# Optimization experiments

Hardware: AMD Instinct MI355X
Metric: run time of the kernel (lower is better)

Reference implementation:

```python
import jax, jax.numpy as jnp
import numpy as np

NEG_SLOPE = 0.2


def gat_layer(x, src, dst, W, a_src, a_dst, b, concat):
    # x: [N, F_in], W: [F_in, H*C], a_src/a_dst: [H, C], b: [H*C] or [C]
    N = x.shape[0]
    H, C = a_src.shape
    h = (x @ W).reshape(N, H, C)                       # per-head projections
    al_s = jnp.einsum('nhc,hc->nh', h, a_src)          # [N, H]
    al_d = jnp.einsum('nhc,hc->nh', h, a_dst)          # [N, H]
    e = jax.nn.leaky_relu(al_s[src] + al_d[dst], NEG_SLOPE)  # [E, H]
    # softmax over incoming edges of each destination node
    m = jax.ops.segment_max(e, dst, num_segments=N)    # [N, H]
    ex = jnp.exp(e - m[dst])
    s = jax.ops.segment_sum(ex, dst, num_segments=N)   # [N, H]
    alpha = ex / (s[dst] + 1e-16)                      # [E, H]
    msg = h[src] * alpha[:, :, None]                   # [E, H, C]
    out = jax.ops.segment_sum(msg, dst, num_segments=N)  # [N, H, C]
    out = out.reshape(N, H * C) if concat else out.mean(axis=1)
    return out + b


def setup_inputs() -> dict:
    key = jax.random.key(0)
    ks = jax.random.split(key, 12)
    N, E, F_in, HID, H, NCLS = 100000, 1600000, 128, 32, 4, 40
    x = jax.random.normal(ks[0], (N, F_in), dtype=jnp.float32)
    edge_index = jax.random.randint(ks[1], (2, E), 0, N, dtype=jnp.int32)
    W1 = jax.random.normal(ks[2], (F_in, H * HID), dtype=jnp.float32) * 0.1
    as1 = jax.random.normal(ks[3], (H, HID), dtype=jnp.float32) * 0.1
    ad1 = jax.random.normal(ks[4], (H, HID), dtype=jnp.float32) * 0.1
    b1 = jnp.zeros((H * HID,), dtype=jnp.float32)
    W2 = jax.random.normal(ks[5], (H * HID, H * NCLS), dtype=jnp.float32) * 0.1
    as2 = jax.random.normal(ks[6], (H, NCLS), dtype=jnp.float32) * 0.1
    ad2 = jax.random.normal(ks[7], (H, NCLS), dtype=jnp.float32) * 0.1
    b2 = jnp.zeros((NCLS,), dtype=jnp.float32)
    return {"x": x, "edge_index": edge_index, "W1": W1, "as1": as1,
            "ad1": ad1, "b1": b1, "W2": W2, "as2": as2, "ad2": ad2, "b2": b2}


def reference(x, edge_index, W1, as1, ad1, b1, W2, as2, ad2, b2):
    src, dst = edge_index[0], edge_index[1]
    h = gat_layer(x, src, dst, W1, as1, ad1, b1, concat=True)
    h = jax.nn.relu(h)  # dropout=0.0 -> identity
    out = gat_layer(h, src, dst, W2, as2, ad2, b2, concat=False)
    return jax.nn.log_softmax(out, axis=-1)
```

## Files before the change

### kernel.cpp

```cpp
#include <hip/hip_runtime.h>

typedef short short8 __attribute__((ext_vector_type(8)));
typedef float f32x4 __attribute__((ext_vector_type(4)));
typedef int   i32x4 __attribute__((ext_vector_type(4)));
typedef unsigned short u16;
typedef unsigned int u32;

__device__ __forceinline__ float b2f(u16 u){ union{u32 i; float f;} v; v.i=((u32)u)<<16; return v.f; }
__device__ __forceinline__ u16 f2b(float f){ union{float f; u32 i;} v; v.f=f; return (u16)((v.i + 0x7fffu + ((v.i>>16)&1u))>>16); }
__device__ __forceinline__ float loadv(const void* p, long i, bool isbf){
  return isbf ? b2f(((const u16*)p)[i]) : ((const float*)p)[i];
}

__global__ void detect_bf16(const void* x, int n, int* flag){
  __shared__ int cnt;
  if (threadIdx.x==0) cnt = 0;
  __syncthreads();
  int m = n < 4096 ? n : 4096;
  int good = 0;
  for (int i = threadIdx.x; i < m; i += 256){
    u16 u = ((const u16*)x)[i];
    int e = (u >> 7) & 0xff;
    if (u == 0 || (e >= 100 && e <= 140)) good++;
  }
  atomicAdd(&cnt, good);
  __syncthreads();
  if (threadIdx.x==0){
    flag[0] = (cnt >= (m*3)/4) ? 1 : 0;
    flag[1] = 1;
  }
}

__global__ __launch_bounds__(256) void convw(const void* __restrict__ W, u16* __restrict__ WT,
                                             int M, const int* __restrict__ flag){
  const bool wbf = *flag != 0;
  int i = blockIdx.x*256 + threadIdx.x;
  if (i >= 128*M) return;
  int k = i / M, c = i - k*M;
  WT[c*128 + k] = wbf ? ((const u16*)W)[i] : f2b(((const float*)W)[i]);
}

__global__ __launch_bounds__(256) void count_x(const int* __restrict__ dst,
    int* __restrict__ counts, int E, int N, int nchunk){
  int r = blockIdx.x & 7;
  int chunk = blockIdx.x >> 3;
  int lo = (int)(((long)N * r) >> 3);
  int hi = (int)(((long)N * (r+1)) >> 3);
  int per = (E + nchunk - 1) / nchunk;
  int s = chunk * per, t = min(E, s + per);
  for (int e = s + threadIdx.x; e < t; e += 256){
    int d = dst[e];
    if (d >= lo && d < hi) atomicAdd(&counts[d], 1);
  }
}

__global__ __launch_bounds__(256) void scatter_x(const int* __restrict__ src, const int* __restrict__ dst,
    const int* __restrict__ rp, int* __restrict__ cur,
    int* __restrict__ psrc, int E, int N, int nchunk){
  int r = blockIdx.x & 7;
  int chunk = blockIdx.x >> 3;
  int lo = (int)(((long)N * r) >> 3);
  int hi = (int)(((long)N * (r+1)) >> 3);
  int per = (E + nchunk - 1) / nchunk;
  int s = chunk * per, t = min(E, s + per);
  for (int e = s + threadIdx.x; e < t; e += 256){
    int d = dst[e];
    if (d >= lo && d < hi){
      int pos = rp[d] + atomicAdd(&cur[d], 1);
      psrc[pos] = src[e];
    }
  }
}

__global__ __launch_bounds__(256) void scan_bsum(const int* __restrict__ counts, int* __restrict__ bsum, int N){
  __shared__ int sm[256];
  int t = threadIdx.x, i = blockIdx.x*256 + t;
  sm[t] = (i < N) ? counts[i] : 0;
  __syncthreads();
  for (int off = 128; off; off >>= 1){
    if (t < off) sm[t] += sm[t+off];
    __syncthreads();
  }
  if (t == 0) bsum[blockIdx.x] = sm[0];
}

__global__ __launch_bounds__(1024) void scan_top(const int* __restrict__ bsum, int* __restrict__ bscan, int B){
  __shared__ int sm[1024];
  int t = threadIdx.x;
  int v = (t < B) ? bsum[t] : 0;
  sm[t] = v;
  __syncthreads();
  for (int off = 1; off < 1024; off <<= 1){
    int x = (t >= off) ? sm[t-off] : 0;
    __syncthreads();
    sm[t] += x;
    __syncthreads();
  }
  if (t < B) bscan[t] = sm[t] - v;
}

__global__ __launch_bounds__(256) void scan_final(const int* __restrict__ counts, const int* __restrict__ bscan,
                                                  int* __restrict__ rp, int N, int E){
  __shared__ int sm[256];
  int t = threadIdx.x, i = blockIdx.x*256 + t;
  int v = (i < N) ? counts[i] : 0;
  sm[t] = v;
  __syncthreads();
  for (int off = 1; off < 256; off <<= 1){
    int x = (t >= off) ? sm[t-off] : 0;
    __syncthreads();
    sm[t] += x;
    __syncthreads();
  }
  if (i < N) rp[i] = bscan[blockIdx.x] + sm[t] - v;
  if (i == 0) rp[N] = E;
}

template<int M>
__global__ __launch_bounds__(256) void gemm_k(const void* __restrict__ X, const u16* __restrict__ WT,
                                              u16* __restrict__ OUT, int N,
                                              const int* __restrict__ flagX){
  __shared__ u16 wt[M][136];
  const bool xbf = *flagX != 0;
  int tid = threadIdx.x;
  for (int i = tid; i < M*16; i += 256){
    int c = i >> 4, k8 = (i & 15) << 3;
    *(short8*)&wt[c][k8] = *(const short8*)&WT[c*128 + k8];
  }
  __syncthreads();
  int wave = tid >> 6, lane = tid & 63;
  int quad = lane >> 4, l16 = lane & 15;
  int rowbase = blockIdx.x*64 + wave*16;
  int rr = rowbase + l16; if (rr >= N) rr = N-1;
  const int NT = M/16;
  f32x4 acc[NT];
  #pragma unroll
  for (int t=0;t<NT;t++) acc[t] = (f32x4){0.f,0.f,0.f,0.f};
  #pragma unroll
  for (int kt = 0; kt < 4; kt++){
    int kb = kt*32 + quad*8;
    short8 a;
    if (xbf){
      a = *(const short8*)((const u16*)X + (size_t)rr*128 + kb);
    } else {
      const float* xf = (const float*)X + (size_t)rr*128 + kb;
      #pragma unroll
      for (int j=0;j<8;j++) a[j] = (short)f2b(xf[j]);
    }
    #pragma unroll
    for (int t=0;t<NT;t++){
      short8 b = *(const short8*)&wt[t*16 + l16][kb];
      acc[t] = __builtin_amdgcn_mfma_f32_16x16x32_bf16(a, b, acc[t], 0, 0, 0);
    }
  }
  #pragma unroll
  for (int t=0;t<NT;t++){
    #pragma unroll
    for (int r=0;r<4;r++){
      int row = rowbase + quad*4 + r;
      if (row < N) OUT[(size_t)row*M + t*16 + l16] = f2b(acc[t][r]);
    }
  }
}

template<int C>
__global__ __launch_bounds__(256) void al_k(const u16* __restrict__ Hm, const void* __restrict__ as_,
                     const void* __restrict__ ad_,
                     float* __restrict__ als, float* __restrict__ ald, int N, const int* __restrict__ flag){
  __shared__ float s_as[4*C], s_ad[4*C];
  const bool isbf = *flag != 0;
  for (int i = threadIdx.x; i < 4*C; i += 256){
    s_as[i] = loadv(as_, i, isbf);
    s_ad[i] = loadv(ad_, i, isbf);
  }
  __syncthreads();
  int idx = blockIdx.x*256 + threadIdx.x;
  if (idx >= N*4) return;
  int n = idx >> 2, h = idx & 3;
  const short8* row = (const short8*)(Hm + (size_t)n*(4*C) + h*C);
  float ss = 0.f, sd = 0.f;
  #pragma unroll
  for (int v = 0; v < C/8; v++){
    short8 pk = row[v];
    #pragma unroll
    for (int j = 0; j < 8; j++){
      union{u32 i; float f;} u; u.i = ((u32)(u16)pk[j]) << 16;
      ss += u.f * s_as[h*C + v*8 + j];
      sd += u.f * s_ad[h*C + v*8 + j];
    }
  }
  als[idx] = ss;
  ald[idx] = sd;
}

__global__ __launch_bounds__(256) void agg1(const u16* __restrict__ h1,
    const float* __restrict__ als, const float* __restrict__ ald, const void* __restrict__ b1,
    const int* __restrict__ rp, const int* __restrict__ psrc,
    u16* __restrict__ hrelu, int N, const int* __restrict__ flag){
  __shared__ __align__(16) int   sbuf[4][16];
  __shared__ __align__(16) float ebT[4][4*20];
  const bool isbf = *flag != 0;
  int wave = threadIdx.x >> 6, lane = threadIdx.x & 63;
  int node = blockIdx.x*4 + wave;
  bool live = node < N;
  int nd = live ? node : 0;
  int hd = lane >> 4;
  int eidx = lane >> 2, hA = lane & 3;
  int beg = __builtin_amdgcn_readfirstlane(rp[nd]);
  int end = __builtin_amdgcn_readfirstlane(rp[nd+1]);
  if (!live){ beg = 0; end = 0; }
  float advA = ald[nd*4 + hA];
  const char* hb = (const char*)h1;
  int lane4 = lane << 2;
  int* sb = sbuf[wave];
  float* eb = ebT[wave];
  float a0 = 0.f, a1 = 0.f;
  float sp = 0.f;
  for (int cbeg = beg; cbeg < end; cbeg += 16){
    int cnt = min(16, end - cbeg);
    int e = cbeg + eidx;
    bool vv = e < end;
    int ec = vv ? e : beg;
    int s = psrc[ec];
    float lv = als[s*4 + hA] + advA;
    lv = fmaxf(lv, 0.2f*lv);
    float ex = vv ? __expf(lv) : 0.f;
    sp += ex;
    eb[hA*20 + eidx] = ex;
    if (hA == 0) sb[eidx] = vv ? (s << 8) : 0;
    for (int j0 = 0; j0 < cnt; j0 += 4){
      i32x4 off4 = *(const i32x4*)&sb[j0];
      f32x4 ex4  = *(const f32x4*)&eb[hd*20 + j0];
      u32 p[4];
      #pragma unroll
      for (int i=0;i<4;i++) p[i] = *(const u32*)(hb + (u32)(off4[i] + lane4));
      #pragma unroll
      for (int i=0;i<4;i++){
        union{u32 u; float f;} w;
        w.u = p[i] << 16;         a0 += ex4[i]*w.f;
        w.u = p[i] & 0xffff0000u; a1 += ex4[i]*w.f;
      }
    }
  }
  sp += __shfl_xor(sp, 4);  sp += __shfl_xor(sp, 8);
  sp += __shfl_xor(sp, 16); sp += __shfl_xor(sp, 32);
  float sum = __shfl(sp, hd);
  if (live){
    float inv = 1.f/(sum + 1e-16f);
    float v0 = a0*inv + loadv(b1, 2*lane,     isbf);
    float v1 = a1*inv + loadv(b1, 2*lane + 1, isbf);
    v0 = v0 > 0.f ? v0 : 0.f;
    v1 = v1 > 0.f ? v1 : 0.f;
    u32 packed = (u32)f2b(v0) | ((u32)f2b(v1) << 16);
    *(u32*)(hrelu + (size_t)node*128 + 2*lane) = packed;
  }
}

__global__ __launch_bounds__(256) void agg2(const u16* __restrict__ h2,
    const float* __restrict__ als, const float* __restrict__ ald, const void* __restrict__ b2,
    const int* __restrict__ rp, const int* __restrict__ psrc,
    void* __restrict__ out, int N, const int* __restrict__ flag){
  __shared__ __align__(16) int   sbuf[4][16];
  __shared__ __align__(16) float ebT[4][4*20];
  __shared__ __align__(16) float sm[4][160];
  const bool isbf = *flag != 0;
  int wave = threadIdx.x >> 6, lane = threadIdx.x & 63;
  int node = blockIdx.x*4 + wave;
  bool live = node < N;
  int nd = live ? node : 0;
  int g = lane >> 4, s = lane & 15;
  int hm = s / 5;
  int moff = s << 4;
  int toff = 256 + (s << 2);
  int eidx = lane >> 2, hA = lane & 3;
  int beg = __builtin_amdgcn_readfirstlane(rp[nd]);
  int end = __builtin_amdgcn_readfirstlane(rp[nd+1]);
  if (!live){ beg = 0; end = 0; }
  float advA = ald[nd*4 + hA];
  const char* hb = (const char*)h2;
  int* sb = sbuf[wave];
  float* eb = ebT[wave];
  float am[8] = {0.f,0.f,0.f,0.f,0.f,0.f,0.f,0.f};
  float at0 = 0.f, at1 = 0.f;
  float sp = 0.f;
  for (int cbeg = beg; cbeg < end; cbeg += 16){
    int cnt = min(16, end - cbeg);
    int e = cbeg + eidx;
    bool vv = e < end;
    int ec = vv ? e : beg;
    int src = psrc[ec];
    float lv = als[src*4 + hA] + advA;
    lv = fmaxf(lv, 0.2f*lv);
    float ex = vv ? __expf(lv) : 0.f;
    sp += ex;
    eb[hA*20 + eidx] = ex;
    if (hA == 0) sb[eidx] = vv ? src*320 : 0;
    for (int j0 = 0; j0 < cnt; j0 += 4){
      int off   = sb[j0 + g];
      float exm = eb[hm*20 + j0 + g];
      float ext = eb[3*20  + j0 + g];
      i32x4 P = *(const i32x4*)(hb + (u32)(off + moff));
      u32   q = *(const u32*) (hb + (u32)(off + toff));
      union{u32 u; float f;} w;
      #pragma unroll
      for (int i=0;i<4;i++){
        u32 pv = (u32)P[i];
        w.u = pv << 16;         am[2*i]   += exm*w.f;
        w.u = pv & 0xffff0000u; am[2*i+1] += exm*w.f;
      }
      w.u = q << 16;         at0 += ext*w.f;
      w.u = q & 0xffff0000u; at1 += ext*w.f;
    }
  }
  sp += __shfl_xor(sp, 4);  sp += __shfl_xor(sp, 8);
  sp += __shfl_xor(sp, 16); sp += __shfl_xor(sp, 32);
  float Sm = __shfl(sp, hm);
  float S3 = __shfl(sp, 3);
  #pragma unroll
  for (int k=0;k<8;k++){ am[k] += __shfl_xor(am[k],16); am[k] += __shfl_xor(am[k],32); }
  at0 += __shfl_xor(at0,16); at0 += __shfl_xor(at0,32);
  at1 += __shfl_xor(at1,16); at1 += __shfl_xor(at1,32);
  if (lane < 16){
    float invm = 1.f/(Sm + 1e-16f);
    float invt = 1.f/(S3 + 1e-16f);
    f32x4 v0 = {am[0]*invm, am[1]*invm, am[2]*invm, am[3]*invm};
    f32x4 v1 = {am[4]*invm, am[5]*invm, am[6]*invm, am[7]*invm};
    *(f32x4*)&sm[wave][8*s]     = v0;
    *(f32x4*)&sm[wave][8*s + 4] = v1;
    sm[wave][128 + 2*s] = at0*invt;
    sm[wave][129 + 2*s] = at1*invt;
  }
  __syncthreads();
  float v = -__builtin_inff();
  if (lane < 40)
    v = (sm[wave][lane] + sm[wave][40+lane] + sm[wave][80+lane] + sm[wave][120+lane]) * 0.25f
        + loadv(b2, lane, isbf);
  float mxo = v;
  for (int o = 32; o; o >>= 1) mxo = fmaxf(mxo, __shfl_xor(mxo, o));
  float ex = (lane < 40) ? __expf(v - mxo) : 0.f;
  float S = ex;
  for (int o = 32; o; o >>= 1) S += __shfl_xor(S, o);
  if (live && lane < 40){
    float r = v - mxo - __logf(S);
    if (isbf) ((u16*)out)[(size_t)node*40 + lane] = f2b(r);
    else      ((float*)out)[(size_t)node*40 + lane] = r;
  }
}

extern "C" void kernel_launch(void* const* d_in, const int* in_sizes, int n_in,
                              void* d_out, int out_size, void* d_ws, size_t ws_size,
                              hipStream_t stream){
  const void* x   = d_in[0];
  const int*  ei  = (const int*)d_in[1];
  const void* W1  = d_in[2];
  const void* as1 = d_in[3];
  const void* ad1 = d_in[4];
  const void* b1  = d_in[5];
  const void* W2  = d_in[6];
  const void* as2 = d_in[7];
  const void* ad2 = d_in[8];
  const void* b2  = d_in[9];

  const int N = in_sizes[0] / 128;
  const int E = in_sizes[1] / 2;
  const int* esrc = ei;
  const int* edst = ei + E;

  char* w = (char*)d_ws;
  size_t off = 0;
  auto take = [&](size_t bytes)->void*{
    void* p = w + off;
    off = (off + bytes + 255) & ~(size_t)255;
    return p;
  };
  u16*   h12    = (u16*)take((size_t)N*160*2);
  u16*   hrelu  = (u16*)take((size_t)N*128*2);
  float* als1   = (float*)take((size_t)N*4*4);
  float* ald1   = (float*)take((size_t)N*4*4);
  float* als2   = (float*)take((size_t)N*4*4);
  float* ald2   = (float*)take((size_t)N*4*4);
  int*   rowptr = (int*)take((size_t)(N+1)*4);
  int*   counts = (int*)take((size_t)N*4);
  int*   bsum   = (int*)take(1024*4);
  int*   bscan  = (int*)take(1024*4);
  int*   psrc   = (int*)take((size_t)E*4);
  int*   flag   = (int*)take(64);
  u16*   wt1    = (u16*)take(128*128*2);
  u16*   wt2    = (u16*)take(160*128*2);

  const int B = (N + 255) / 256;
  const int NCHUNK = 128;

  detect_bf16<<<1, 256, 0, stream>>>(x, N*128, flag);
  convw<<<(128*128+255)/256, 256, 0, stream>>>(W1, wt1, 128, flag);
  convw<<<(128*160+255)/256, 256, 0, stream>>>(W2, wt2, 160, flag);

  hipMemsetAsync(counts, 0, (size_t)N*4, stream);
  count_x<<<8*NCHUNK, 256, 0, stream>>>(edst, counts, E, N, NCHUNK);
  scan_bsum<<<B, 256, 0, stream>>>(counts, bsum, N);
  scan_top<<<1, 1024, 0, stream>>>(bsum, bscan, B);
  scan_final<<<B, 256, 0, stream>>>(counts, bscan, rowptr, N, E);
  hipMemsetAsync(counts, 0, (size_t)N*4, stream);
  scatter_x<<<8*NCHUNK, 256, 0, stream>>>(esrc, edst, rowptr, counts, psrc, E, N, NCHUNK);

  gemm_k<128><<<(N+63)/64, 256, 0, stream>>>(x, wt1, h12, N, flag);
  al_k<32><<<(4*N+255)/256, 256, 0, stream>>>(h12, as1, ad1, als1, ald1, N, flag);
  agg1<<<(N+3)/4, 256, 0, stream>>>(h12, als1, ald1, b1, rowptr, psrc, hrelu, N, flag);

  gemm_k<160><<<(N+63)/64, 256, 0, stream>>>(hrelu, wt2, h12, N, flag+1);
  al_k<40><<<(4*N+255)/256, 256, 0, stream>>>(h12, as2, ad2, als2, ald2, N, flag);
  agg2<<<(N+3)/4, 256, 0, stream>>>(h12, als2, ald2, b2, rowptr, psrc, d_out, N, flag);
}
```

Measured before the change: 486.8 us.

## Split edge softmax numerators into separate kernel and batch gathers in aggregation

Adds an edgex kernel that computes the per-edge exp scores and per-node denominators ahead of time and stores them in a workspace buffer. The aggregation kernels then just read the precomputed values. agg1 is remapped to 16-byte row loads with a cross-group reduction like agg2. Both aggregations now issue four gathers at once on full 16-edge chunks to raise memory-level parallelism. The cost is an extra launch plus writing and reading a 25.6 MB edge buffer for each layer.

```diff
diff --git a/kernel.cpp b/kernel.cpp
--- a/kernel.cpp
+++ b/kernel.cpp
@@ -193,75 +193,119 @@
   ald[idx] = sd;
 }
 
+__global__ __launch_bounds__(256) void edgex(const float* __restrict__ als, const float* __restrict__ ald,
+    const int* __restrict__ rp, const int* __restrict__ psrc,
+    float* __restrict__ ex, float* __restrict__ nsum, int N){
+  int wave = threadIdx.x >> 6, lane = threadIdx.x & 63;
+  int node = blockIdx.x*4 + wave;
+  bool live = node < N;
+  int nd = live ? node : 0;
+  int eidx = lane >> 2, hA = lane & 3;
+  int beg = __builtin_amdgcn_readfirstlane(rp[nd]);
+  int end = __builtin_amdgcn_readfirstlane(rp[nd+1]);
+  if (!live){ beg = 0; end = 0; }
+  float adv = ald[nd*4 + hA];
+  float sp = 0.f;
+  for (int cbeg = beg; cbeg < end; cbeg += 16){
+    int e = cbeg + eidx;
+    if (e < end){
+      int s = psrc[e];
+      float lv = als[s*4 + hA] + adv;
+      lv = fmaxf(lv, 0.2f*lv);
+      float ev = __expf(lv);
+      sp += ev;
+      ex[(size_t)e*4 + hA] = ev;
+    }
+  }
+  sp += __shfl_xor(sp, 4);  sp += __shfl_xor(sp, 8);
+  sp += __shfl_xor(sp, 16); sp += __shfl_xor(sp, 32);
+  if (live && lane < 4) nsum[nd*4 + lane] = sp;
+}
+
 __global__ __launch_bounds__(256) void agg1(const u16* __restrict__ h1,
-    const float* __restrict__ als, const float* __restrict__ ald, const void* __restrict__ b1,
+    const float* __restrict__ ex, const float* __restrict__ nsum, const void* __restrict__ b1,
     const int* __restrict__ rp, const int* __restrict__ psrc,
     u16* __restrict__ hrelu, int N, const int* __restrict__ flag){
   __shared__ __align__(16) int   sbuf[4][16];
-  __shared__ __align__(16) float ebT[4][4*20];
+  __shared__ __align__(16) float ebuf[4][64];
   const bool isbf = *flag != 0;
   int wave = threadIdx.x >> 6, lane = threadIdx.x & 63;
   int node = blockIdx.x*4 + wave;
   bool live = node < N;
   int nd = live ? node : 0;
-  int hd = lane >> 4;
+  int g = lane >> 4, s = lane & 15;
+  int hm = s >> 2;
+  int moff = s << 4;
   int eidx = lane >> 2, hA = lane & 3;
   int beg = __builtin_amdgcn_readfirstlane(rp[nd]);
   int end = __builtin_amdgcn_readfirstlane(rp[nd+1]);
   if (!live){ beg = 0; end = 0; }
-  float advA = ald[nd*4 + hA];
   const char* hb = (const char*)h1;
-  int lane4 = lane << 2;
   int* sb = sbuf[wave];
-  float* eb = ebT[wave];
-  float a0 = 0.f, a1 = 0.f;
-  float sp = 0.f;
+  float* eb = ebuf[wave];
+  float am[8] = {0.f,0.f,0.f,0.f,0.f,0.f,0.f,0.f};
   for (int cbeg = beg; cbeg < end; cbeg += 16){
     int cnt = min(16, end - cbeg);
     int e = cbeg + eidx;
     bool vv = e < end;
-    int ec = vv ? e : beg;
-    int s = psrc[ec];
-    float lv = als[s*4 + hA] + advA;
-    lv = fmaxf(lv, 0.2f*lv);
-    float ex = vv ? __expf(lv) : 0.f;
-    sp += ex;
-    eb[hA*20 + eidx] = ex;
-    if (hA == 0) sb[eidx] = vv ? (s << 8) : 0;
-    for (int j0 = 0; j0 < cnt; j0 += 4){
-      i32x4 off4 = *(const i32x4*)&sb[j0];
-      f32x4 ex4  = *(const f32x4*)&eb[hd*20 + j0];
-      u32 p[4];
-      #pragma unroll
-      for (int i=0;i<4;i++) p[i] = *(const u32*)(hb + (u32)(off4[i] + lane4));
-      #pragma unroll
-      for (int i=0;i<4;i++){
+    float exv = vv ? ex[(size_t)e*4 + hA] : 0.f;
+    eb[lane] = exv;
+    if (hA == 0) sb[eidx] = vv ? (psrc[e] << 8) : 0;
+    int njj = (cnt + 3) >> 2;
+    if (njj == 4){
+      int of[4]; float em[4]; i32x4 P[4];
+      #pragma unroll
+      for (int jj=0;jj<4;jj++){ of[jj] = sb[jj*4 + g]; em[jj] = eb[(jj*4 + g)*4 + hm]; }
+      #pragma unroll
+      for (int jj=0;jj<4;jj++) P[jj] = *(const i32x4*)(hb + (u32)(of[jj] + moff));
+      #pragma unroll
+      for (int jj=0;jj<4;jj++){
         union{u32 u; float f;} w;
-        w.u = p[i] << 16;         a0 += ex4[i]*w.f;
-        w.u = p[i] & 0xffff0000u; a1 += ex4[i]*w.f;
-      }
-    }
-  }
-  sp += __shfl_xor(sp, 4);  sp += __shfl_xor(sp, 8);
-  sp += __shfl_xor(sp, 16); sp += __shfl_xor(sp, 32);
-  float sum = __shfl(sp, hd);
-  if (live){
-    float inv = 1.f/(sum + 1e-16f);
-    float v0 = a0*inv + loadv(b1, 2*lane,     isbf);
-    float v1 = a1*inv + loadv(b1, 2*lane + 1, isbf);
-    v0 = v0 > 0.f ? v0 : 0.f;
-    v1 = v1 > 0.f ? v1 : 0.f;
-    u32 packed = (u32)f2b(v0) | ((u32)f2b(v1) << 16);
-    *(u32*)(hrelu + (size_t)node*128 + 2*lane) = packed;
+        #pragma unroll
+        for (int i=0;i<4;i++){
+          u32 pv = (u32)P[jj][i];
+          w.u = pv << 16;         am[2*i]   += em[jj]*w.f;
+          w.u = pv & 0xffff0000u; am[2*i+1] += em[jj]*w.f;
+        }
+      }
+    } else {
+      for (int jj=0;jj<njj;jj++){
+        int of = sb[jj*4 + g]; float em = eb[(jj*4 + g)*4 + hm];
+        i32x4 P = *(const i32x4*)(hb + (u32)(of + moff));
+        union{u32 u; float f;} w;
+        #pragma unroll
+        for (int i=0;i<4;i++){
+          u32 pv = (u32)P[i];
+          w.u = pv << 16;         am[2*i]   += em*w.f;
+          w.u = pv & 0xffff0000u; am[2*i+1] += em*w.f;
+        }
+      }
+    }
+  }
+  #pragma unroll
+  for (int k=0;k<8;k++){ am[k] += __shfl_xor(am[k],16); am[k] += __shfl_xor(am[k],32); }
+  if (live && lane < 16){
+    float Sm = nsum[nd*4 + hm];
+    float inv = 1.f/(Sm + 1e-16f);
+    float v[8];
+    #pragma unroll
+    for (int k=0;k<8;k++){
+      float t = am[k]*inv + loadv(b1, 8*s + k, isbf);
+      v[k] = t > 0.f ? t : 0.f;
+    }
+    i32x4 pk;
+    #pragma unroll
+    for (int k=0;k<4;k++) pk[k] = (int)((u32)f2b(v[2*k]) | ((u32)f2b(v[2*k+1]) << 16));
+    *(i32x4*)(hrelu + (size_t)node*128 + 8*s) = pk;
   }
 }
 
 __global__ __launch_bounds__(256) void agg2(const u16* __restrict__ h2,
-    const float* __restrict__ als, const float* __restrict__ ald, const void* __restrict__ b2,
+    const float* __restrict__ ex, const float* __restrict__ nsum, const void* __restrict__ b2,
     const int* __restrict__ rp, const int* __restrict__ psrc,
     void* __restrict__ out, int N, const int* __restrict__ flag){
   __shared__ __align__(16) int   sbuf[4][16];
-  __shared__ __align__(16) float ebT[4][4*20];
+  __shared__ __align__(16) float ebuf[4][64];
   __shared__ __align__(16) float sm[4][160];
   const bool isbf = *flag != 0;
   int wave = threadIdx.x >> 6, lane = threadIdx.x & 63;
@@ -276,51 +320,70 @@
   int beg = __builtin_amdgcn_readfirstlane(rp[nd]);
   int end = __builtin_amdgcn_readfirstlane(rp[nd+1]);
   if (!live){ beg = 0; end = 0; }
-  float advA = ald[nd*4 + hA];
   const char* hb = (const char*)h2;
   int* sb = sbuf[wave];
-  float* eb = ebT[wave];
+  float* eb = ebuf[wave];
   float am[8] = {0.f,0.f,0.f,0.f,0.f,0.f,0.f,0.f};
   float at0 = 0.f, at1 = 0.f;
-  float sp = 0.f;
   for (int cbeg = beg; cbeg < end; cbeg += 16){
     int cnt = min(16, end - cbeg);
     int e = cbeg + eidx;
     bool vv = e < end;
-    int ec = vv ? e : beg;
-    int src = psrc[ec];
-    float lv = als[src*4 + hA] + advA;
-    lv = fmaxf(lv, 0.2f*lv);
-    float ex = vv ? __expf(lv) : 0.f;
-    sp += ex;
-    eb[hA*20 + eidx] = ex;
-    if (hA == 0) sb[eidx] = vv ? src*320 : 0;
-    for (int j0 = 0; j0 < cnt; j0 += 4){
-      int off   = sb[j0 + g];
-      float exm = eb[hm*20 + j0 + g];
-      float ext = eb[3*20  + j0 + g];
-      i32x4 P = *(const i32x4*)(hb + (u32)(off + moff));
-      u32   q = *(const u32*) (hb + (u32)(off + toff));
-      union{u32 u; float f;} w;
-      #pragma unroll
-      for (int i=0;i<4;i++){
-        u32 pv = (u32)P[i];
-        w.u = pv << 16;         am[2*i]   += exm*w.f;
-        w.u = pv & 0xffff0000u; am[2*i+1] += exm*w.f;
-      }
-      w.u = q << 16;         at0 += ext*w.f;
-      w.u = q & 0xffff0000u; at1 += ext*w.f;
-    }
-  }
-  sp += __shfl_xor(sp, 4);  sp += __shfl_xor(sp, 8);
-  sp += __shfl_xor(sp, 16); sp += __shfl_xor(sp, 32);
-  float Sm = __shfl(sp, hm);
-  float S3 = __shfl(sp, 3);
+    float exv = vv ? ex[(size_t)e*4 + hA] : 0.f;
+    eb[lane] = exv;
+    if (hA == 0) sb[eidx] = vv ? psrc[e]*320 : 0;
+    int njj = (cnt + 3) >> 2;
+    if (njj == 4){
+      int of[4]; float em[4], et[4]; i32x4 P[4]; u32 q[4];
+      #pragma unroll
+      for (int jj=0;jj<4;jj++){
+        of[jj] = sb[jj*4 + g];
+        em[jj] = eb[(jj*4 + g)*4 + hm];
+        et[jj] = eb[(jj*4 + g)*4 + 3];
+      }
+      #pragma unroll
+      for (int jj=0;jj<4;jj++){
+        P[jj] = *(const i32x4*)(hb + (u32)(of[jj] + moff));
+        q[jj] = *(const u32*) (hb + (u32)(of[jj] + toff));
+      }
+      #pragma unroll
+      for (int jj=0;jj<4;jj++){
+        union{u32 u; float f;} w;
+        #pragma unroll
+        for (int i=0;i<4;i++){
+          u32 pv = (u32)P[jj][i];
+          w.u = pv << 16;         am[2*i]   += em[jj]*w.f;
+          w.u = pv & 0xffff0000u; am[2*i+1] += em[jj]*w.f;
+        }
+        w.u = q[jj] << 16;         at0 += et[jj]*w.f;
+        w.u = q[jj] & 0xffff0000u; at1 += et[jj]*w.f;
+      }
+    } else {
+      for (int jj=0;jj<njj;jj++){
+        int of = sb[jj*4 + g];
+        float em = eb[(jj*4 + g)*4 + hm];
+        float et = eb[(jj*4 + g)*4 + 3];
+        i32x4 P = *(const i32x4*)(hb + (u32)(of + moff));
+        u32   q = *(const u32*) (hb + (u32)(of + toff));
+        union{u32 u; float f;} w;
+        #pragma unroll
+        for (int i=0;i<4;i++){
+          u32 pv = (u32)P[i];
+          w.u = pv << 16;         am[2*i]   += em*w.f;
+          w.u = pv & 0xffff0000u; am[2*i+1] += em*w.f;
+        }
+        w.u = q << 16;         at0 += et*w.f;
+        w.u = q & 0xffff0000u; at1 += et*w.f;
+      }
+    }
+  }
   #pragma unroll
   for (int k=0;k<8;k++){ am[k] += __shfl_xor(am[k],16); am[k] += __shfl_xor(am[k],32); }
   at0 += __shfl_xor(at0,16); at0 += __shfl_xor(at0,32);
   at1 += __shfl_xor(at1,16); at1 += __shfl_xor(at1,32);
   if (lane < 16){
+    float Sm = nsum[nd*4 + hm];
+    float S3 = nsum[nd*4 + 3];
     float invm = 1.f/(Sm + 1e-16f);
     float invt = 1.f/(S3 + 1e-16f);
     f32x4 v0 = {am[0]*invm, am[1]*invm, am[2]*invm, am[3]*invm};
@@ -337,8 +400,8 @@
         + loadv(b2, lane, isbf);
   float mxo = v;
   for (int o = 32; o; o >>= 1) mxo = fmaxf(mxo, __shfl_xor(mxo, o));
-  float ex = (lane < 40) ? __expf(v - mxo) : 0.f;
-  float S = ex;
+  float exl = (lane < 40) ? __expf(v - mxo) : 0.f;
+  float S = exl;
   for (int o = 32; o; o >>= 1) S += __shfl_xor(S, o);
   if (live && lane < 40){
     float r = v - mxo - __logf(S);
@@ -387,6 +450,8 @@
   int*   flag   = (int*)take(64);
   u16*   wt1    = (u16*)take(128*128*2);
   u16*   wt2    = (u16*)take(160*128*2);
+  float* exbuf  = (float*)take((size_t)E*4*4);
+  float* nsum   = (float*)take((size_t)N*4*4);
 
   const int B = (N + 255) / 256;
   const int NCHUNK = 128;
@@ -405,9 +470,11 @@
 
   gemm_k<128><<<(N+63)/64, 256, 0, stream>>>(x, wt1, h12, N, flag);
   al_k<32><<<(4*N+255)/256, 256, 0, stream>>>(h12, as1, ad1, als1, ald1, N, flag);
-  agg1<<<(N+3)/4, 256, 0, stream>>>(h12, als1, ald1, b1, rowptr, psrc, hrelu, N, flag);
+  edgex<<<(N+3)/4, 256, 0, stream>>>(als1, ald1, rowptr, psrc, exbuf, nsum, N);
+  agg1<<<(N+3)/4, 256, 0, stream>>>(h12, exbuf, nsum, b1, rowptr, psrc, hrelu, N, flag);
 
   gemm_k<160><<<(N+63)/64, 256, 0, stream>>>(hrelu, wt2, h12, N, flag+1);
   al_k<40><<<(4*N+255)/256, 256, 0, stream>>>(h12, as2, ad2, als2, ald2, N, flag);
-  agg2<<<(N+3)/4, 256, 0, stream>>>(h12, als2, ald2, b2, rowptr, psrc, d_out, N, flag);
-}
+  edgex<<<(N+3)/4, 256, 0, stream>>>(als2, ald2, rowptr, psrc, exbuf, nsum, N);
+  agg2<<<(N+3)/4, 256, 0, stream>>>(h12, exbuf, nsum, b2, rowptr, psrc, d_out, N, flag);
+}
```

New measurement: 534.1 us. +9.7%, slower.

## Split layer-2 features into 128+32 arrays and single-pass CSR build

Applied to the files above, without the earlier changes.

Layer-2 projected features are now stored as a 128-wide main array plus a separate 32-wide tail array instead of one 160-wide interleaved array. The gather in agg2 reads each 16-byte chunk from a 256-byte aligned row plus a 4-byte tail read from a 64-byte row, which should improve cache-line alignment for the random neighbor loads. The count and scatter kernels drop the 8-way destination-range partitioning and do one pass over the edges with a grid-stride loop. That removes the 8x redundant edge reads but gives up whatever atomic locality the partitioning provided.

```diff
diff --git a/kernel.cpp b/kernel.cpp
--- a/kernel.cpp
+++ b/kernel.cpp
@@ -40,35 +40,20 @@
   WT[c*128 + k] = wbf ? ((const u16*)W)[i] : f2b(((const float*)W)[i]);
 }
 
-__global__ __launch_bounds__(256) void count_x(const int* __restrict__ dst,
-    int* __restrict__ counts, int E, int N, int nchunk){
-  int r = blockIdx.x & 7;
-  int chunk = blockIdx.x >> 3;
-  int lo = (int)(((long)N * r) >> 3);
-  int hi = (int)(((long)N * (r+1)) >> 3);
-  int per = (E + nchunk - 1) / nchunk;
-  int s = chunk * per, t = min(E, s + per);
-  for (int e = s + threadIdx.x; e < t; e += 256){
+__global__ __launch_bounds__(256) void count_1p(const int* __restrict__ dst, int* __restrict__ counts, int E){
+  int i = blockIdx.x*256 + threadIdx.x;
+  int stride = gridDim.x*256;
+  for (int e = i; e < E; e += stride) atomicAdd(&counts[dst[e]], 1);
+}
+
+__global__ __launch_bounds__(256) void scatter_1p(const int* __restrict__ src, const int* __restrict__ dst,
+    const int* __restrict__ rp, int* __restrict__ cur, int* __restrict__ psrc, int E){
+  int i = blockIdx.x*256 + threadIdx.x;
+  int stride = gridDim.x*256;
+  for (int e = i; e < E; e += stride){
     int d = dst[e];
-    if (d >= lo && d < hi) atomicAdd(&counts[d], 1);
-  }
-}
-
-__global__ __launch_bounds__(256) void scatter_x(const int* __restrict__ src, const int* __restrict__ dst,
-    const int* __restrict__ rp, int* __restrict__ cur,
-    int* __restrict__ psrc, int E, int N, int nchunk){
-  int r = blockIdx.x & 7;
-  int chunk = blockIdx.x >> 3;
-  int lo = (int)(((long)N * r) >> 3);
-  int hi = (int)(((long)N * (r+1)) >> 3);
-  int per = (E + nchunk - 1) / nchunk;
-  int s = chunk * per, t = min(E, s + per);
-  for (int e = s + threadIdx.x; e < t; e += 256){
-    int d = dst[e];
-    if (d >= lo && d < hi){
-      int pos = rp[d] + atomicAdd(&cur[d], 1);
-      psrc[pos] = src[e];
-    }
+    int pos = rp[d] + atomicAdd(&cur[d], 1);
+    psrc[pos] = src[e];
   }
 }
 
@@ -118,7 +103,7 @@
 
 template<int M>
 __global__ __launch_bounds__(256) void gemm_k(const void* __restrict__ X, const u16* __restrict__ WT,
-                                              u16* __restrict__ OUT, int N,
+                                              u16* __restrict__ OUT, u16* __restrict__ OUT2, int N,
                                               const int* __restrict__ flagX){
   __shared__ u16 wt[M][136];
   const bool xbf = *flagX != 0;
@@ -158,7 +143,11 @@
     #pragma unroll
     for (int r=0;r<4;r++){
       int row = rowbase + quad*4 + r;
-      if (row < N) OUT[(size_t)row*M + t*16 + l16] = f2b(acc[t][r]);
+      if (row < N){
+        u16 val = f2b(acc[t][r]);
+        if (M > 128 && t*16 >= 128) OUT2[(size_t)row*32 + (t*16 - 128) + l16] = val;
+        else                        OUT [(size_t)row*128 + t*16 + l16]        = val;
+      }
     }
   }
 }
@@ -187,6 +176,37 @@
       union{u32 i; float f;} u; u.i = ((u32)(u16)pk[j]) << 16;
       ss += u.f * s_as[h*C + v*8 + j];
       sd += u.f * s_ad[h*C + v*8 + j];
+    }
+  }
+  als[idx] = ss;
+  ald[idx] = sd;
+}
+
+__global__ __launch_bounds__(256) void al2_k(const u16* __restrict__ Hm, const u16* __restrict__ Ht,
+                     const void* __restrict__ as_, const void* __restrict__ ad_,
+                     float* __restrict__ als, float* __restrict__ ald, int N, const int* __restrict__ flag){
+  __shared__ float s_as[160], s_ad[160];
+  const bool isbf = *flag != 0;
+  for (int i = threadIdx.x; i < 160; i += 256){
+    s_as[i] = loadv(as_, i, isbf);
+    s_ad[i] = loadv(ad_, i, isbf);
+  }
+  __syncthreads();
+  int idx = blockIdx.x*256 + threadIdx.x;
+  if (idx >= N*4) return;
+  int n = idx >> 2, h = idx & 3;
+  float ss = 0.f, sd = 0.f;
+  int c0 = h*40;
+  #pragma unroll
+  for (int v = 0; v < 5; v++){
+    int c = c0 + v*8;
+    const u16* p = (c < 128) ? (Hm + (size_t)n*128 + c) : (Ht + (size_t)n*32 + (c - 128));
+    short8 pk = *(const short8*)p;
+    #pragma unroll
+    for (int j = 0; j < 8; j++){
+      union{u32 i; float f;} u; u.i = ((u32)(u16)pk[j]) << 16;
+      ss += u.f * s_as[c + j];
+      sd += u.f * s_ad[c + j];
     }
   }
   als[idx] = ss;
@@ -256,7 +276,7 @@
   }
 }
 
-__global__ __launch_bounds__(256) void agg2(const u16* __restrict__ h2,
+__global__ __launch_bounds__(256) void agg2(const u16* __restrict__ h2m, const u16* __restrict__ h2t,
     const float* __restrict__ als, const float* __restrict__ ald, const void* __restrict__ b2,
     const int* __restrict__ rp, const int* __restrict__ psrc,
     void* __restrict__ out, int N, const int* __restrict__ flag){
@@ -271,13 +291,14 @@
   int g = lane >> 4, s = lane & 15;
   int hm = s / 5;
   int moff = s << 4;
-  int toff = 256 + (s << 2);
+  int tof  = s << 2;
   int eidx = lane >> 2, hA = lane & 3;
   int beg = __builtin_amdgcn_readfirstlane(rp[nd]);
   int end = __builtin_amdgcn_readfirstlane(rp[nd+1]);
   if (!live){ beg = 0; end = 0; }
   float advA = ald[nd*4 + hA];
-  const char* hb = (const char*)h2;
+  const char* hbm = (const char*)h2m;
+  const char* hbt = (const char*)h2t;
   int* sb = sbuf[wave];
   float* eb = ebT[wave];
   float am[8] = {0.f,0.f,0.f,0.f,0.f,0.f,0.f,0.f};
@@ -294,13 +315,13 @@
     float ex = vv ? __expf(lv) : 0.f;
     sp += ex;
     eb[hA*20 + eidx] = ex;
-    if (hA == 0) sb[eidx] = vv ? src*320 : 0;
+    if (hA == 0) sb[eidx] = vv ? src : 0;
     for (int j0 = 0; j0 < cnt; j0 += 4){
-      int off   = sb[j0 + g];
+      int sv    = sb[j0 + g];
       float exm = eb[hm*20 + j0 + g];
       float ext = eb[3*20  + j0 + g];
-      i32x4 P = *(const i32x4*)(hb + (u32)(off + moff));
-      u32   q = *(const u32*) (hb + (u32)(off + toff));
+      i32x4 P = *(const i32x4*)(hbm + ((((u32)sv) << 8) + moff));
+      u32   q = *(const u32*) (hbt + ((((u32)sv) << 6) + tof));
       union{u32 u; float f;} w;
       #pragma unroll
       for (int i=0;i<4;i++){
@@ -337,8 +358,8 @@
         + loadv(b2, lane, isbf);
   float mxo = v;
   for (int o = 32; o; o >>= 1) mxo = fmaxf(mxo, __shfl_xor(mxo, o));
-  float ex = (lane < 40) ? __expf(v - mxo) : 0.f;
-  float S = ex;
+  float exl = (lane < 40) ? __expf(v - mxo) : 0.f;
+  float S = exl;
   for (int o = 32; o; o >>= 1) S += __shfl_xor(S, o);
   if (live && lane < 40){
     float r = v - mxo - __logf(S);
@@ -373,7 +394,8 @@
     off = (off + bytes + 255) & ~(size_t)255;
     return p;
   };
-  u16*   h12    = (u16*)take((size_t)N*160*2);
+  u16*   h12    = (u16*)take((size_t)N*128*2);
+  u16*   h2t    = (u16*)take((size_t)N*32*2);
   u16*   hrelu  = (u16*)take((size_t)N*128*2);
   float* als1   = (float*)take((size_t)N*4*4);
   float* ald1   = (float*)take((size_t)N*4*4);
@@ -389,25 +411,24 @@
   u16*   wt2    = (u16*)take(160*128*2);
 
   const int B = (N + 255) / 256;
-  const int NCHUNK = 128;
 
   detect_bf16<<<1, 256, 0, stream>>>(x, N*128, flag);
   convw<<<(128*128+255)/256, 256, 0, stream>>>(W1, wt1, 128, flag);
   convw<<<(128*160+255)/256, 256, 0, stream>>>(W2, wt2, 160, flag);
 
   hipMemsetAsync(counts, 0, (size_t)N*4, stream);
-  count_x<<<8*NCHUNK, 256, 0, stream>>>(edst, counts, E, N, NCHUNK);
+  count_1p<<<2048, 256, 0, stream>>>(edst, counts, E);
   scan_bsum<<<B, 256, 0, stream>>>(counts, bsum, N);
   scan_top<<<1, 1024, 0, stream>>>(bsum, bscan, B);
   scan_final<<<B, 256, 0, stream>>>(counts, bscan, rowptr, N, E);
   hipMemsetAsync(counts, 0, (size_t)N*4, stream);
-  scatter_x<<<8*NCHUNK, 256, 0, stream>>>(esrc, edst, rowptr, counts, psrc, E, N, NCHUNK);
-
-  gemm_k<128><<<(N+63)/64, 256, 0, stream>>>(x, wt1, h12, N, flag);
+  scatter_1p<<<2048, 256, 0, stream>>>(esrc, edst, rowptr, counts, psrc, E);
+
+  gemm_k<128><<<(N+63)/64, 256, 0, stream>>>(x, wt1, h12, h2t , N, flag);
   al_k<32><<<(4*N+255)/256, 256, 0, stream>>>(h12, as1, ad1, als1, ald1, N, flag);
   agg1<<<(N+3)/4, 256, 0, stream>>>(h12, als1, ald1, b1, rowptr, psrc, hrelu, N, flag);
 
-  gemm_k<160><<<(N+63)/64, 256, 0, stream>>>(hrelu, wt2, h12, N, flag+1);
-  al_k<40><<<(4*N+255)/256, 256, 0, stream>>>(h12, as2, ad2, als2, ald2, N, flag);
-  agg2<<<(N+3)/4, 256, 0, stream>>>(h12, als2, ald2, b2, rowptr, psrc, d_out, N, flag);
-}
+  gemm_k<160><<<(N+63)/64, 256, 0, stream>>>(hrelu, wt2, h12, h2t, N, flag+1);
+  al2_k<<<(4*N+255)/256, 256, 0, stream>>>(h12, h2t, as2, ad2, als2, ald2, N, flag);
+  agg2<<<(N+3)/4, 256, 0, stream>>>(h12, h2t, als2, ald2, b2, rowptr, psrc, d_out, N, flag);
+}
```

Measured after the change: 526.7 us. 8.2% more time.
